# Kernel optimization log

Measured on AMD Instinct MI355X. Metric: run time of the kernel, lower is better.

Reference implementation:

```python
import jax, jax.numpy as jnp
import numpy as np


def setup_inputs() -> dict:
    key = jax.random.key(0)
    k1, k2, k3, k4 = jax.random.split(key, 4)
    c = 256
    x = jax.random.normal(k1, (4, c, 64, 64), dtype=jnp.float32)
    # 1x1 conv weights act as channel-mixing matrices
    w_qkv = jax.random.normal(k2, (3 * c, c), dtype=jnp.float32) * (1.0 / np.sqrt(c))
    w_out = jax.random.normal(k3, (c, c), dtype=jnp.float32) * (1.0 / np.sqrt(c))
    b_out = jax.random.normal(k4, (c,), dtype=jnp.float32) * 0.01
    return {"x": x, "w_qkv": w_qkv, "w_out": w_out, "b_out": b_out}


def reference(x, w_qkv, w_out, b_out):
    b, c, h, w = x.shape
    heads = 4
    d = c // heads
    scale = d ** (-0.5)
    hw = h * w

    # 1x1 conv (no bias): [b,3c,h,w]
    qkv = jnp.einsum('oc,bchw->bohw', w_qkv, x)
    q, k, v = jnp.split(qkv, 3, axis=1)

    def to_seq(t):
        # [b,c,h,w] -> [b,heads,hw,d]
        return t.reshape(b, heads, d, hw).transpose(0, 1, 3, 2)

    q, k, v = to_seq(q), to_seq(k), to_seq(v)

    sim = jnp.einsum('bhid,bhjd->bhij', q, k) * scale
    attn = jax.nn.softmax(sim, axis=-1)
    out = jnp.einsum('bhij,bhjd->bhid', attn, v)

    # [b,heads,hw,d] -> [b,c,h,w]
    out = out.transpose(0, 1, 3, 2).reshape(b, c, h, w)

    # output 1x1 conv with bias, plus residual
    proj = jnp.einsum('oc,bchw->bohw', w_out, out) + b_out[None, :, None, None]
    return x + proj
```

## Files before the change

### kernel.cpp

```cpp
#include <hip/hip_runtime.h>


#define HW 4096
#define CIN 256
#define LOG2E_DIV8 0.18033688011112042f
#define SM_SHIFT 8.0f

typedef __attribute__((ext_vector_type(8))) short short8v;
typedef __attribute__((ext_vector_type(4))) short short4v;
typedef __attribute__((ext_vector_type(4))) float float4v;
typedef __attribute__((ext_vector_type(16))) float f32x16;
typedef __attribute__((ext_vector_type(4))) unsigned int uint4v;

typedef const __attribute__((address_space(1))) unsigned int* gptr_t;
typedef __attribute__((address_space(3))) unsigned int* lptr_t;

static __device__ __forceinline__ unsigned short f2bf(float f) {
    unsigned int u = __float_as_uint(f);
    u += 0x7fff + ((u >> 16) & 1);
    return (unsigned short)(u >> 16);
}
static __device__ __forceinline__ float bf2f(unsigned short v) {
    return __uint_as_float((unsigned int)v << 16);
}
static __device__ __forceinline__ unsigned int pkbf(float a, float b) {
    unsigned int r;
    asm("v_cvt_pk_bf16_f32 %0, %1, %2" : "=v"(r) : "v"(a), "v"(b));
    return r;
}
static __device__ __forceinline__ void pl32swap(unsigned int& a, unsigned int& b) {
    asm volatile("v_permlane32_swap_b32 %0, %1" : "+v"(a), "+v"(b));
}

__global__ __launch_bounds__(256) void cast_all_k(
    const float* __restrict__ w_qkv, const float* __restrict__ w_out,
    const float* __restrict__ x,
    unsigned short* __restrict__ wqb, unsigned short* __restrict__ wob,
    unsigned short* __restrict__ xt)
{
    const int bi = blockIdx.x;
    const int t = threadIdx.x;
    __shared__ float tile[64][65];

    if (bi < 192) {
        const int idx = bi * 1024 + t * 4;
        const float s = (idx < 256 * 256) ? LOG2E_DIV8 : 1.0f;
        const float4 v = *(const float4*)&w_qkv[idx];
        uint2 pk;
        pk.x = pkbf(v.x * s, v.y * s);
        pk.y = pkbf(v.z * s, v.w * s);
        *(uint2*)&wqb[idx] = pk;
    } else if (bi < 256) {
        const int idx = (bi - 192) * 1024 + t * 4;
        const float4 v = *(const float4*)&w_out[idx];
        uint2 pk;
        pk.x = pkbf(v.x, v.y);
        pk.y = pkbf(v.z, v.w);
        *(uint2*)&wob[idx] = pk;
    } else {
        const int bx = bi - 256;
        const int p0 = (bx & 63) * 64;
        const int c0 = ((bx >> 6) & 3) * 64;
        const int b  = bx >> 8;

        const float* xb = x + ((size_t)b * CIN + c0) * HW + p0;
        #pragma unroll
        for (int iter = 0; iter < 4; ++iter) {
            const int idx = iter * 1024 + t * 4;
            const int cc = idx >> 6, pp = idx & 63;
            const float4 v = *(const float4*)&xb[(size_t)cc * HW + pp];
            tile[cc][pp + 0] = v.x; tile[cc][pp + 1] = v.y;
            tile[cc][pp + 2] = v.z; tile[cc][pp + 3] = v.w;
        }
        __syncthreads();
        unsigned short* xo = xt + ((size_t)b * HW + p0) * CIN + c0;
        #pragma unroll
        for (int iter = 0; iter < 4; ++iter) {
            const int idx = iter * 1024 + t * 4;
            const int pp = idx >> 6, cc = idx & 63;
            uint2 pk;
            pk.x = pkbf(tile[cc + 0][pp], tile[cc + 1][pp]);
            pk.y = pkbf(tile[cc + 2][pp], tile[cc + 3][pp]);
            *(uint2*)&xo[(size_t)pp * CIN + cc] = pk;
        }
    }
}

__global__ __launch_bounds__(256) void qkv_mfma_k(
    const unsigned short* __restrict__ wqb, const unsigned short* __restrict__ xt,
    unsigned short* __restrict__ qb, unsigned short* __restrict__ kb,
    unsigned short* __restrict__ vb)
{
    const int o0 = blockIdx.x * 128;
    const int p0 = blockIdx.y * 128;
    const int b  = blockIdx.z;
    const int t = threadIdx.x;
    const int wid = t >> 6, lane = t & 63, g = lane >> 4, li = lane & 15;
    const int wo = (wid >> 1) * 64, wp = (wid & 1) * 64;

    __shared__ char alds[16384];
    __shared__ char blds[16384];

    const int srow8 = t >> 3, sc16 = t & 7;
    const char* asrc = (const char*)wqb + ((size_t)(o0 + srow8) * 256) * 2 + sc16 * 16;
    const char* bsrc = (const char*)xt + (((size_t)b * HW + p0 + srow8) * 256) * 2 + sc16 * 16;

    float4 areg[4], breg[4];
    #pragma unroll
    for (int it = 0; it < 4; ++it) {
        areg[it] = *(const float4*)(asrc + (size_t)it * 32 * 512);
        breg[it] = *(const float4*)(bsrc + (size_t)it * 32 * 512);
    }

    float4v acc[4][4];
    #pragma unroll
    for (int mt = 0; mt < 4; ++mt)
        #pragma unroll
        for (int nt = 0; nt < 4; ++nt) acc[mt][nt] = (float4v){0.f, 0.f, 0.f, 0.f};

    for (int ks = 0; ks < 4; ++ks) {
        #pragma unroll
        for (int it = 0; it < 4; ++it) {
            const int row = it * 32 + srow8;
            const int dsw = row * 128 + ((sc16 * 16) ^ ((row & 7) << 4));
            *(float4*)(alds + dsw) = areg[it];
            *(float4*)(blds + dsw) = breg[it];
        }
        __syncthreads();
        if (ks < 3) {
            #pragma unroll
            for (int it = 0; it < 4; ++it) {
                areg[it] = *(const float4*)(asrc + (size_t)it * 32 * 512 + (ks + 1) * 128);
                breg[it] = *(const float4*)(bsrc + (size_t)it * 32 * 512 + (ks + 1) * 128);
            }
        }
        short8v af[4][2], bf[4][2];
        #pragma unroll
        for (int mt = 0; mt < 4; ++mt) {
            const int row = wo + mt * 16 + li;
            #pragma unroll
            for (int kc = 0; kc < 2; ++kc)
                af[mt][kc] = *(const short8v*)(alds + row * 128 + ((kc * 64 + g * 16) ^ ((row & 7) << 4)));
        }
        #pragma unroll
        for (int nt = 0; nt < 4; ++nt) {
            const int row = wp + nt * 16 + li;
            #pragma unroll
            for (int kc = 0; kc < 2; ++kc)
                bf[nt][kc] = *(const short8v*)(blds + row * 128 + ((kc * 64 + g * 16) ^ ((row & 7) << 4)));
        }
        #pragma unroll
        for (int mt = 0; mt < 4; ++mt)
            #pragma unroll
            for (int nt = 0; nt < 4; ++nt) {
                acc[mt][nt] = __builtin_amdgcn_mfma_f32_16x16x32_bf16(af[mt][0], bf[nt][0], acc[mt][nt], 0, 0, 0);
                acc[mt][nt] = __builtin_amdgcn_mfma_f32_16x16x32_bf16(af[mt][1], bf[nt][1], acc[mt][nt], 0, 0, 0);
            }
        __syncthreads();
    }

    const int which = o0 >> 8;
    #pragma unroll
    for (int mt = 0; mt < 4; ++mt) {
        const int o_b = o0 + wo + mt * 16 + g * 4;
        const int head = (o_b >> 6) & 3;
        const int dd = o_b & 63;
        const int bh = b * 4 + head;
        if (which < 2) {
            unsigned short* dst = which ? kb : qb;
            #pragma unroll
            for (int nt = 0; nt < 4; ++nt) {
                const int p = p0 + wp + nt * 16 + li;
                uint2 pk;
                pk.x = pkbf(acc[mt][nt][0], acc[mt][nt][1]);
                pk.y = pkbf(acc[mt][nt][2], acc[mt][nt][3]);
                *(uint2*)&dst[((size_t)bh * HW + p) * 64 + dd] = pk;
            }
        } else {
            #pragma unroll
            for (int nt = 0; nt < 4; ++nt) {
                const int p = p0 + wp + nt * 16 + li;
                #pragma unroll
                for (int r = 0; r < 4; ++r)
                    vb[((size_t)bh * 64 + dd + r) * HW + p] = f2bf(acc[mt][nt][r]);
            }
        }
    }
}

__global__ __launch_bounds__(256, 4) void flash_mfma_k(
    const unsigned short* __restrict__ qb, const unsigned short* __restrict__ kb,
    const unsigned short* __restrict__ vb, unsigned short* __restrict__ po,
    float* __restrict__ pl)
{
    const int i0 = blockIdx.x * 128;
    const int bh = blockIdx.y;
    const int sp = blockIdx.z;
    const int t = threadIdx.x;
    const int wid = t >> 6, lane = t & 63;
    const int q32 = lane & 31, hi = lane >> 5;

    const unsigned short* qg = qb + (size_t)bh * HW * 64;
    const unsigned short* kg = kb + (size_t)bh * HW * 64 + (size_t)sp * 2048 * 64;
    const unsigned short* vg = vb + (size_t)bh * 64 * HW + (size_t)sp * 2048;

    __shared__ char klds[2][8192];
    __shared__ char vlds[2][8192];

    const int q = i0 + wid * 32 + q32;
    short8v qf[4];
    #pragma unroll
    for (int kc = 0; kc < 4; ++kc)
        qf[kc] = *(const short8v*)(qg + (size_t)q * 64 + kc * 16 + hi * 8);

    float l = 0.f;
    f32x16 acco[2];
    f32x16 accs[2];
    short8v pf[2][2];
    #pragma unroll
    for (int r = 0; r < 16; ++r) { acco[0][r] = 0.f; acco[1][r] = 0.f; }

    const int srow = t >> 3;
    const int scol = (t & 7) * 16;
    const int ssw  = (srow & 7) << 4;
    const char* kgsrc0 = (const char*)kg + (size_t)srow * 128 + (scol ^ ssw);
    const char* kgsrc1 = kgsrc0 + 32 * 128;
    const char* vgsrc0 = (const char*)vg + (size_t)srow * 8192 + (scol ^ ssw);
    const char* vgsrc1 = vgsrc0 + (size_t)32 * 8192;

    auto ISSUE = [&](int tile, int buf) {
        __builtin_amdgcn_global_load_lds(
            (gptr_t)(kgsrc0 + (size_t)tile * 8192),
            (lptr_t)(klds[buf] + t * 16), 16, 0, 0);
        __builtin_amdgcn_global_load_lds(
            (gptr_t)(kgsrc1 + (size_t)tile * 8192),
            (lptr_t)(klds[buf] + 4096 + t * 16), 16, 0, 0);
        __builtin_amdgcn_global_load_lds(
            (gptr_t)(vgsrc0 + (size_t)tile * 128),
            (lptr_t)(vlds[buf] + t * 16), 16, 0, 0);
        __builtin_amdgcn_global_load_lds(
            (gptr_t)(vgsrc1 + (size_t)tile * 128),
            (lptr_t)(vlds[buf] + 4096 + t * 16), 16, 0, 0);
    };
    auto SMM = [&](int buf) {
        #pragma unroll
        for (int r = 0; r < 16; ++r) { accs[0][r] = -SM_SHIFT; accs[1][r] = -SM_SHIFT; }
        __builtin_amdgcn_s_setprio(1);
        #pragma unroll
        for (int jt = 0; jt < 2; ++jt) {
            const int row = jt * 32 + q32;
            const char* kbase = klds[buf] + row * 128;
            const int sw = (row & 7) << 4;
            #pragma unroll
            for (int kc = 0; kc < 4; ++kc) {
                const short8v kf = *(const short8v*)(kbase + ((kc * 32 + hi * 16) ^ sw));
                accs[jt] = __builtin_amdgcn_mfma_f32_32x32x16_bf16(kf, qf[kc], accs[jt], 0, 0, 0);
            }
        }
        __builtin_amdgcn_s_setprio(0);
    };
    auto SOFT = [&]() {
        float ls = 0.f;
        #pragma unroll
        for (int jt = 0; jt < 2; ++jt) {
            float p[16];
            #pragma unroll
            for (int r = 0; r < 16; ++r) p[r] = __builtin_amdgcn_exp2f(accs[jt][r]);
            float s0 = (p[0] + p[1]) + (p[2] + p[3]);
            float s1 = (p[4] + p[5]) + (p[6] + p[7]);
            float s2 = (p[8] + p[9]) + (p[10] + p[11]);
            float s3 = (p[12] + p[13]) + (p[14] + p[15]);
            ls += (s0 + s1) + (s2 + s3);
            unsigned int w0 = pkbf(p[0], p[1]);
            unsigned int w1 = pkbf(p[2], p[3]);
            unsigned int w2 = pkbf(p[4], p[5]);
            unsigned int w3 = pkbf(p[6], p[7]);
            pl32swap(w0, w2);
            pl32swap(w1, w3);
            uint4v fa; fa[0] = w0; fa[1] = w1; fa[2] = w2; fa[3] = w3;
            pf[jt][0] = __builtin_bit_cast(short8v, fa);
            unsigned int w4_ = pkbf(p[8],  p[9]);
            unsigned int w5 = pkbf(p[10], p[11]);
            unsigned int w6 = pkbf(p[12], p[13]);
            unsigned int w7 = pkbf(p[14], p[15]);
            pl32swap(w4_, w6);
            pl32swap(w5, w7);
            uint4v fb; fb[0] = w4_; fb[1] = w5; fb[2] = w6; fb[3] = w7;
            pf[jt][1] = __builtin_bit_cast(short8v, fb);
        }
        l += ls;
    };
    auto PVMM = [&](int buf) {
        __builtin_amdgcn_s_setprio(1);
        #pragma unroll
        for (int dt = 0; dt < 2; ++dt) {
            const int row = dt * 32 + q32;
            const char* vbase = vlds[buf] + row * 128;
            const int sw = (row & 7) << 4;
            #pragma unroll
            for (int jt = 0; jt < 2; ++jt)
                #pragma unroll
                for (int kr = 0; kr < 2; ++kr) {
                    const short8v vf = *(const short8v*)(vbase + ((jt * 64 + kr * 32 + hi * 16) ^ sw));
                    acco[dt] = __builtin_amdgcn_mfma_f32_32x32x16_bf16(vf, pf[jt][kr], acco[dt], 0, 0, 0);
                }
        }
        __builtin_amdgcn_s_setprio(0);
    };

    ISSUE(0, 0);
    __syncthreads();

    int buf = 0;
    for (int kt = 0; kt < 32; ++kt) {
        if (kt < 31) ISSUE(kt + 1, buf ^ 1);
        SMM(buf);
        SOFT();
        PVMM(buf);
        __syncthreads();
        buf ^= 1;
    }

    const float ltot = l + __shfl_xor(l, 32, 64);
    unsigned short* prow = po + ((size_t)(sp * 16 + bh) * HW + q) * 64;
    #pragma unroll
    for (int dt = 0; dt < 2; ++dt)
        #pragma unroll
        for (int g4 = 0; g4 < 4; ++g4) {
            const int d0 = dt * 32 + 8 * g4 + 4 * hi;
            uint2 pk;
            pk.x = pkbf(acco[dt][g4 * 4 + 0], acco[dt][g4 * 4 + 1]);
            pk.y = pkbf(acco[dt][g4 * 4 + 2], acco[dt][g4 * 4 + 3]);
            *(uint2*)&prow[d0] = pk;
        }
    if (hi == 0) pl[(size_t)(sp * 16 + bh) * HW + q] = ltot;
}

__global__ __launch_bounds__(256) void combine_k(
    const unsigned short* __restrict__ po, const float* __restrict__ pl,
    unsigned short* __restrict__ att)
{
    const int gid = blockIdx.x * 256 + threadIdx.x;
    const int half = gid & 1;
    const int q = (gid >> 1) & 4095;
    const int bh = gid >> 13;
    const int b = bh >> 2, head = bh & 3;

    const size_t r0 = (size_t)bh * HW + q;
    const size_t r1 = (size_t)(16 + bh) * HW + q;
    const float inv = 1.0f / (pl[r0] + pl[r1]);

    const unsigned short* p0 = po + r0 * 64 + half * 32;
    const unsigned short* p1 = po + r1 * 64 + half * 32;
    unsigned short* ao = att + ((size_t)b * HW + q) * CIN + head * 64 + half * 32;

    #pragma unroll
    for (int w = 0; w < 4; ++w) {
        const short8v a = *(const short8v*)(p0 + w * 8);
        const short8v c = *(const short8v*)(p1 + w * 8);
        uint4v r;
        #pragma unroll
        for (int i = 0; i < 4; ++i) {
            const float lo = (bf2f((unsigned short)a[2 * i])     + bf2f((unsigned short)c[2 * i]))     * inv;
            const float hv = (bf2f((unsigned short)a[2 * i + 1]) + bf2f((unsigned short)c[2 * i + 1])) * inv;
            r[i] = pkbf(lo, hv);
        }
        *(uint4v*)(ao + w * 8) = r;
    }
}

__global__ __launch_bounds__(256) void proj_mfma_k(
    const unsigned short* __restrict__ wob, const unsigned short* __restrict__ att,
    const float* __restrict__ bias, const float* __restrict__ x,
    float* __restrict__ out)
{
    const int o0 = blockIdx.x * 128;
    const int p0 = blockIdx.y * 128;
    const int b  = blockIdx.z;
    const int t = threadIdx.x;
    const int wid = t >> 6, lane = t & 63, g = lane >> 4, li = lane & 15;
    const int wo = (wid >> 1) * 64, wp = (wid & 1) * 64;

    __shared__ char alds[16384];
    __shared__ char blds[16384];

    const int srow8 = t >> 3, sc16 = t & 7;
    const char* asrc = (const char*)wob + ((size_t)(o0 + srow8) * 256) * 2 + sc16 * 16;
    const char* bsrc = (const char*)att + (((size_t)b * HW + p0 + srow8) * 256) * 2 + sc16 * 16;

    float4 areg[4], breg[4];
    #pragma unroll
    for (int it = 0; it < 4; ++it) {
        areg[it] = *(const float4*)(asrc + (size_t)it * 32 * 512);
        breg[it] = *(const float4*)(bsrc + (size_t)it * 32 * 512);
    }

    float4v acc[4][4];
    #pragma unroll
    for (int mt = 0; mt < 4; ++mt)
        #pragma unroll
        for (int nt = 0; nt < 4; ++nt) acc[mt][nt] = (float4v){0.f, 0.f, 0.f, 0.f};

    for (int ks = 0; ks < 4; ++ks) {
        #pragma unroll
        for (int it = 0; it < 4; ++it) {
            const int row = it * 32 + srow8;
            const int dsw = row * 128 + ((sc16 * 16) ^ ((row & 7) << 4));
            *(float4*)(alds + dsw) = areg[it];
            *(float4*)(blds + dsw) = breg[it];
        }
        __syncthreads();
        if (ks < 3) {
            #pragma unroll
            for (int it = 0; it < 4; ++it) {
                areg[it] = *(const float4*)(asrc + (size_t)it * 32 * 512 + (ks + 1) * 128);
                breg[it] = *(const float4*)(bsrc + (size_t)it * 32 * 512 + (ks + 1) * 128);
            }
        }
        short8v af[4][2], bf[4][2];
        #pragma unroll
        for (int mt = 0; mt < 4; ++mt) {
            const int row = wo + mt * 16 + li;
            #pragma unroll
            for (int kc = 0; kc < 2; ++kc)
                af[mt][kc] = *(const short8v*)(alds + row * 128 + ((kc * 64 + g * 16) ^ ((row & 7) << 4)));
        }
        #pragma unroll
        for (int nt = 0; nt < 4; ++nt) {
            const int row = wp + nt * 16 + li;
            #pragma unroll
            for (int kc = 0; kc < 2; ++kc)
                bf[nt][kc] = *(const short8v*)(blds + row * 128 + ((kc * 64 + g * 16) ^ ((row & 7) << 4)));
        }
        #pragma unroll
        for (int mt = 0; mt < 4; ++mt)
            #pragma unroll
            for (int nt = 0; nt < 4; ++nt) {
                acc[mt][nt] = __builtin_amdgcn_mfma_f32_16x16x32_bf16(af[mt][0], bf[nt][0], acc[mt][nt], 0, 0, 0);
                acc[mt][nt] = __builtin_amdgcn_mfma_f32_16x16x32_bf16(af[mt][1], bf[nt][1], acc[mt][nt], 0, 0, 0);
            }
        __syncthreads();
    }

    #pragma unroll
    for (int mt = 0; mt < 4; ++mt) {
        const int o_b = o0 + wo + mt * 16 + g * 4;
        #pragma unroll
        for (int nt = 0; nt < 4; ++nt) {
            const int p = p0 + wp + nt * 16 + li;
            #pragma unroll
            for (int r = 0; r < 4; ++r) {
                const int o = o_b + r;
                const size_t ix = ((size_t)b * CIN + o) * HW + p;
                out[ix] = acc[mt][nt][r] + bias[o] + x[ix];
            }
        }
    }
}

extern "C" void kernel_launch(void* const* d_in, const int* in_sizes, int n_in,
                              void* d_out, int out_size, void* d_ws, size_t ws_size,
                              hipStream_t stream)
{
    const float* x     = (const float*)d_in[0];
    const float* w_qkv = (const float*)d_in[1];
    const float* w_out = (const float*)d_in[2];
    const float* b_out = (const float*)d_in[3];
    float* out = (float*)d_out;

    char* ws = (char*)d_ws;
    const size_t MB = 1024 * 1024;
    unsigned short* xt  = (unsigned short*)(ws);
    unsigned short* qb  = (unsigned short*)(ws + 8 * MB);
    unsigned short* kb  = (unsigned short*)(ws + 16 * MB);
    unsigned short* vb  = (unsigned short*)(ws + 24 * MB);
    unsigned short* att = (unsigned short*)(ws + 32 * MB);
    unsigned short* wqb = (unsigned short*)(ws + 40 * MB);
    unsigned short* wob = (unsigned short*)(ws + 40 * MB + 768 * 256 * 2);
    unsigned short* po  = (unsigned short*)(ws + 41 * MB);
    float*          pl  = (float*)(ws + 57 * MB);

    cast_all_k<<<1280, 256, 0, stream>>>(w_qkv, w_out, x, wqb, wob, xt);
    qkv_mfma_k<<<dim3(6, 32, 4), 256, 0, stream>>>(wqb, xt, qb, kb, vb);
    flash_mfma_k<<<dim3(32, 16, 2), 256, 0, stream>>>(qb, kb, vb, po, pl);
    combine_k<<<512, 256, 0, stream>>>(po, pl, att);
    proj_mfma_k<<<dim3(2, 32, 4), 256, 0, stream>>>(wob, att, b_out, x, out);
}
```

Measured before the change: 144.6 us.

## Fuse split-KV combine into output projection and merge score/softmax stages

Removes the separate combine kernel: the projection kernel now loads both split-KV partial outputs and row sums directly, normalizes and packs them to bf16 while staging the B operand. This drops one launch and the write and re-read of the intermediate attention buffer. The flash kernel also computes scores per 32-key tile and applies exp immediately, instead of holding both score accumulators live, which may lower register pressure. In exchange, each projection block redundantly reloads the row sums and does a division per row, and the two output-channel blocks (grid x=2) both repeat the combine arithmetic.

```diff
diff --git a/kernel.cpp b/kernel.cpp
--- a/kernel.cpp
+++ b/kernel.cpp
@@ -215,7 +215,6 @@
 
     float l = 0.f;
     f32x16 acco[2];
-    f32x16 accs[2];
     short8v pf[2][2];
     #pragma unroll
     for (int r = 0; r < 16; ++r) { acco[0][r] = 0.f; acco[1][r] = 0.f; }
@@ -242,30 +241,26 @@
             (gptr_t)(vgsrc1 + (size_t)tile * 128),
             (lptr_t)(vlds[buf] + 4096 + t * 16), 16, 0, 0);
     };
-    auto SMM = [&](int buf) {
-        #pragma unroll
-        for (int r = 0; r < 16; ++r) { accs[0][r] = -SM_SHIFT; accs[1][r] = -SM_SHIFT; }
-        __builtin_amdgcn_s_setprio(1);
+    auto SSOFT = [&](int buf) {
+        float ls = 0.f;
         #pragma unroll
         for (int jt = 0; jt < 2; ++jt) {
+            f32x16 s;
+            #pragma unroll
+            for (int r = 0; r < 16; ++r) s[r] = -SM_SHIFT;
             const int row = jt * 32 + q32;
             const char* kbase = klds[buf] + row * 128;
             const int sw = (row & 7) << 4;
+            __builtin_amdgcn_s_setprio(1);
             #pragma unroll
             for (int kc = 0; kc < 4; ++kc) {
                 const short8v kf = *(const short8v*)(kbase + ((kc * 32 + hi * 16) ^ sw));
-                accs[jt] = __builtin_amdgcn_mfma_f32_32x32x16_bf16(kf, qf[kc], accs[jt], 0, 0, 0);
-            }
-        }
-        __builtin_amdgcn_s_setprio(0);
-    };
-    auto SOFT = [&]() {
-        float ls = 0.f;
-        #pragma unroll
-        for (int jt = 0; jt < 2; ++jt) {
+                s = __builtin_amdgcn_mfma_f32_32x32x16_bf16(kf, qf[kc], s, 0, 0, 0);
+            }
+            __builtin_amdgcn_s_setprio(0);
             float p[16];
             #pragma unroll
-            for (int r = 0; r < 16; ++r) p[r] = __builtin_amdgcn_exp2f(accs[jt][r]);
+            for (int r = 0; r < 16; ++r) p[r] = __builtin_amdgcn_exp2f(s[r]);
             float s0 = (p[0] + p[1]) + (p[2] + p[3]);
             float s1 = (p[4] + p[5]) + (p[6] + p[7]);
             float s2 = (p[8] + p[9]) + (p[10] + p[11]);
@@ -314,8 +309,7 @@
     int buf = 0;
     for (int kt = 0; kt < 32; ++kt) {
         if (kt < 31) ISSUE(kt + 1, buf ^ 1);
-        SMM(buf);
-        SOFT();
+        SSOFT(buf);
         PVMM(buf);
         __syncthreads();
         buf ^= 1;
@@ -336,43 +330,10 @@
     if (hi == 0) pl[(size_t)(sp * 16 + bh) * HW + q] = ltot;
 }
 
-__global__ __launch_bounds__(256) void combine_k(
-    const unsigned short* __restrict__ po, const float* __restrict__ pl,
-    unsigned short* __restrict__ att)
-{
-    const int gid = blockIdx.x * 256 + threadIdx.x;
-    const int half = gid & 1;
-    const int q = (gid >> 1) & 4095;
-    const int bh = gid >> 13;
-    const int b = bh >> 2, head = bh & 3;
-
-    const size_t r0 = (size_t)bh * HW + q;
-    const size_t r1 = (size_t)(16 + bh) * HW + q;
-    const float inv = 1.0f / (pl[r0] + pl[r1]);
-
-    const unsigned short* p0 = po + r0 * 64 + half * 32;
-    const unsigned short* p1 = po + r1 * 64 + half * 32;
-    unsigned short* ao = att + ((size_t)b * HW + q) * CIN + head * 64 + half * 32;
-
-    #pragma unroll
-    for (int w = 0; w < 4; ++w) {
-        const short8v a = *(const short8v*)(p0 + w * 8);
-        const short8v c = *(const short8v*)(p1 + w * 8);
-        uint4v r;
-        #pragma unroll
-        for (int i = 0; i < 4; ++i) {
-            const float lo = (bf2f((unsigned short)a[2 * i])     + bf2f((unsigned short)c[2 * i]))     * inv;
-            const float hv = (bf2f((unsigned short)a[2 * i + 1]) + bf2f((unsigned short)c[2 * i + 1])) * inv;
-            r[i] = pkbf(lo, hv);
-        }
-        *(uint4v*)(ao + w * 8) = r;
-    }
-}
-
 __global__ __launch_bounds__(256) void proj_mfma_k(
-    const unsigned short* __restrict__ wob, const unsigned short* __restrict__ att,
-    const float* __restrict__ bias, const float* __restrict__ x,
-    float* __restrict__ out)
+    const unsigned short* __restrict__ wob, const unsigned short* __restrict__ po,
+    const float* __restrict__ pl, const float* __restrict__ bias,
+    const float* __restrict__ x, float* __restrict__ out)
 {
     const int o0 = blockIdx.x * 128;
     const int p0 = blockIdx.y * 128;
@@ -386,13 +347,30 @@
 
     const int srow8 = t >> 3, sc16 = t & 7;
     const char* asrc = (const char*)wob + ((size_t)(o0 + srow8) * 256) * 2 + sc16 * 16;
-    const char* bsrc = (const char*)att + (((size_t)b * HW + p0 + srow8) * 256) * 2 + sc16 * 16;
+
+    auto loadB = [&](int it, int ks) -> float4 {
+        const int p = p0 + srow8 + it * 32;
+        const int bh = b * 4 + ks;
+        const size_t r0 = (size_t)bh * HW + p;
+        const size_t r1 = (size_t)(16 + bh) * HW + p;
+        const short8v a = *(const short8v*)(po + r0 * 64 + sc16 * 8);
+        const short8v c = *(const short8v*)(po + r1 * 64 + sc16 * 8);
+        const float inv = 1.0f / (pl[r0] + pl[r1]);
+        uint4v rr;
+        #pragma unroll
+        for (int i = 0; i < 4; ++i) {
+            const float lo = (bf2f((unsigned short)a[2 * i])     + bf2f((unsigned short)c[2 * i]))     * inv;
+            const float hv = (bf2f((unsigned short)a[2 * i + 1]) + bf2f((unsigned short)c[2 * i + 1])) * inv;
+            rr[i] = pkbf(lo, hv);
+        }
+        return __builtin_bit_cast(float4, rr);
+    };
 
     float4 areg[4], breg[4];
     #pragma unroll
     for (int it = 0; it < 4; ++it) {
         areg[it] = *(const float4*)(asrc + (size_t)it * 32 * 512);
-        breg[it] = *(const float4*)(bsrc + (size_t)it * 32 * 512);
+        breg[it] = loadB(it, 0);
     }
 
     float4v acc[4][4];
@@ -414,7 +392,7 @@
             #pragma unroll
             for (int it = 0; it < 4; ++it) {
                 areg[it] = *(const float4*)(asrc + (size_t)it * 32 * 512 + (ks + 1) * 128);
-                breg[it] = *(const float4*)(bsrc + (size_t)it * 32 * 512 + (ks + 1) * 128);
+                breg[it] = loadB(it, ks + 1);
             }
         }
         short8v af[4][2], bf[4][2];
@@ -474,7 +452,6 @@
     unsigned short* qb  = (unsigned short*)(ws + 8 * MB);
     unsigned short* kb  = (unsigned short*)(ws + 16 * MB);
     unsigned short* vb  = (unsigned short*)(ws + 24 * MB);
-    unsigned short* att = (unsigned short*)(ws + 32 * MB);
     unsigned short* wqb = (unsigned short*)(ws + 40 * MB);
     unsigned short* wob = (unsigned short*)(ws + 40 * MB + 768 * 256 * 2);
     unsigned short* po  = (unsigned short*)(ws + 41 * MB);
@@ -483,6 +460,5 @@
     cast_all_k<<<1280, 256, 0, stream>>>(w_qkv, w_out, x, wqb, wob, xt);
     qkv_mfma_k<<<dim3(6, 32, 4), 256, 0, stream>>>(wqb, xt, qb, kb, vb);
     flash_mfma_k<<<dim3(32, 16, 2), 256, 0, stream>>>(qb, kb, vb, po, pl);
-    combine_k<<<512, 256, 0, stream>>>(po, pl, att);
-    proj_mfma_k<<<dim3(2, 32, 4), 256, 0, stream>>>(wob, att, b_out, x, out);
-}
+    proj_mfma_k<<<dim3(2, 32, 4), 256, 0, stream>>>(wob, po, pl, b_out, x, out);
+}
```

Measured after the change: 265.5 us. 83.5% more time.
